# Kernel optimization log

Hardware: AMD Instinct MI355X
Metric: run time of the kernel (lower is better)

## Reference

```python
import jax, jax.numpy as jnp
import numpy as np

N = 50000          # node_num
E = 800000         # edges before self-loops (avg degree 16)
H = 1              # heads
C = 64             # out_channel (== embedding dim)
D_IN = 64          # in_channel
NEG_SLOPE = 0.2    # GraphLayer leaky_relu negative_slope
BN_EPS = 1e-5


def setup_inputs() -> dict:
    key = jax.random.key(0)
    ks = jax.random.split(key, 12)
    x = jax.random.normal(ks[0], (N, D_IN), jnp.float32)
    # random edges with no self-loops (forward removes then re-adds self-loops)
    src = jax.random.randint(ks[1], (E,), 0, N, dtype=jnp.int32)
    off = jax.random.randint(ks[2], (E,), 1, N, dtype=jnp.int32)
    dst = (src + off) % N
    edge_index = jnp.stack([src, dst])            # [2, E], row0=j (source), row1=i (target)
    embedding = jax.random.normal(ks[3], (N, C), jnp.float32)
    sc = 1.0 / np.sqrt(D_IN)
    W = jax.random.normal(ks[4], (H * C, D_IN), jnp.float32) * sc   # lin.weight
    att_i = jax.random.normal(ks[5], (1, H, C), jnp.float32) * 0.1
    att_j = jax.random.normal(ks[6], (1, H, C), jnp.float32) * 0.1
    att_em_i = jax.random.normal(ks[7], (1, H, C), jnp.float32) * 0.1
    att_em_j = jax.random.normal(ks[8], (1, H, C), jnp.float32) * 0.1
    bias = jnp.zeros((C,), jnp.float32)           # GraphLayer bias (concat=False)
    bn_gamma = jnp.ones((C,), jnp.float32)
    bn_beta = jnp.zeros((C,), jnp.float32)
    return {"x": x, "edge_index": edge_index, "embedding": embedding, "W": W,
            "att_i": att_i, "att_j": att_j, "att_em_i": att_em_i, "att_em_j": att_em_j,
            "bias": bias, "bn_gamma": bn_gamma, "bn_beta": bn_beta}


def reference(x, edge_index, embedding, W, att_i, att_j, att_em_i, att_em_j, bias, bn_gamma, bn_beta):
    n = x.shape[0]
    xl = (x @ W.T).reshape(n, H, C)                       # lin(x) -> [N, H, C]
    # add self-loops (input edges have none)
    loops = jnp.arange(n, dtype=edge_index.dtype)
    src = jnp.concatenate([edge_index[0], loops])         # j
    dst = jnp.concatenate([edge_index[1], loops])         # i (aggregation target)
    x_j = xl[src]                                         # [E', H, C]
    x_i = xl[dst]
    emb_i = embedding[dst][:, None, :]                    # [E', 1, C] broadcast over heads
    emb_j = embedding[src][:, None, :]
    # alpha = <cat(x_i, emb_i), cat(att_i, att_em_i)> + <cat(x_j, emb_j), cat(att_j, att_em_j)>
    a = ((x_i * att_i).sum(-1) + (emb_i * att_em_i).sum(-1)
         + (x_j * att_j).sum(-1) + (emb_j * att_em_j).sum(-1))   # [E', H]
    a = jnp.where(a >= 0, a, NEG_SLOPE * a)               # leaky_relu(0.2)
    # segment softmax over target nodes
    amax = jax.ops.segment_max(a, dst, num_segments=n)    # every node has a self-loop
    ea = jnp.exp(a - amax[dst])
    denom = jax.ops.segment_sum(ea, dst, num_segments=n)
    alpha = ea / (denom[dst] + 1e-16)                     # [E', H]
    msg = x_j * alpha[..., None]                          # [E', H, C]
    out = jax.ops.segment_sum(msg, dst, num_segments=n)   # [N, H, C]
    out = out.mean(axis=1) + bias                         # concat=False -> head mean
    # BatchNorm1d (training mode: batch stats) + ReLU
    mu = out.mean(axis=0)
    var = ((out - mu) ** 2).mean(axis=0)
    out = (out - mu) * jax.lax.rsqrt(var + BN_EPS) * bn_gamma + bn_beta
    return jnp.maximum(out, 0.0)
```

## Files before the change

### kernel.cpp

```cpp
#include <hip/hip_runtime.h>
#include <hip/hip_bf16.h>

#define NEG_SLOPE 0.2f
#define BN_EPS 1e-5f
#define CAP 48
#define NGRP 391
#define NSLICE 782
#define PER 1024
#define SLICELEN 1024

typedef __attribute__((ext_vector_type(8))) short bf16x8;
typedef __attribute__((ext_vector_type(4))) float f32x4;
typedef __attribute__((ext_vector_type(4))) int i32x4;

__device__ __forceinline__ bf16x8 pk8(float4 a, float4 b) {
    union { __hip_bfloat16 h; short s; } u;
    bf16x8 r;
    u.h = __float2bfloat16(a.x); r[0] = u.s;
    u.h = __float2bfloat16(a.y); r[1] = u.s;
    u.h = __float2bfloat16(a.z); r[2] = u.s;
    u.h = __float2bfloat16(a.w); r[3] = u.s;
    u.h = __float2bfloat16(b.x); r[4] = u.s;
    u.h = __float2bfloat16(b.y); r[5] = u.s;
    u.h = __float2bfloat16(b.z); r[6] = u.s;
    u.h = __float2bfloat16(b.w); r[7] = u.s;
    return r;
}

__global__ void __launch_bounds__(256, 8)
k_part_mfma(const float* __restrict__ x, const float* __restrict__ W,
            const float* __restrict__ emb,
            const float* __restrict__ att_i, const float* __restrict__ att_j,
            const float* __restrict__ att_em_i, const float* __restrict__ att_em_j,
            const int* __restrict__ src, const int* __restrict__ dst, int E,
            unsigned* __restrict__ region, unsigned short* __restrict__ start16,
            __hip_bfloat16* __restrict__ xlh, float* __restrict__ s_i,
            float* __restrict__ s_j, float* __restrict__ sums, int N) {
    __shared__ unsigned cnt[NGRP];
    __shared__ unsigned pfx[NGRP + 1];
    __shared__ unsigned run[NGRP];
    __shared__ unsigned sbuf[PER];
    int tid = threadIdx.x;
    int lane = tid & 63;
    int m = lane & 15;
    int q = lane >> 4;

    if (blockIdx.x == 0 && tid < 128) sums[tid] = 0.f;

    int gw = blockIdx.x * 4 + (tid >> 6);
    int ntiles = (N + 15) >> 4;
    int r0 = gw * 16;
    int rload = r0 + m; if (rload > N - 1) rload = N - 1;
    const float* xrow = x + (size_t)rload * 64;
    float4 xa0 = *(const float4*)(xrow + q * 8);
    float4 xa1 = *(const float4*)(xrow + q * 8 + 4);
    float4 xb0 = *(const float4*)(xrow + 32 + q * 8);
    float4 xb1 = *(const float4*)(xrow + 32 + q * 8 + 4);

    {
        int b = blockIdx.x;
        int e0 = b * PER;
        int e1 = e0 + PER; if (e1 > E) e1 = E;
        int ecnt = e1 - e0; if (ecnt < 0) ecnt = 0;
        int e4 = ecnt & ~3;
        for (int gg = tid; gg < NGRP; gg += 256) cnt[gg] = 0;
        __syncthreads();
        int o = tid * 4;
        i32x4 d4 = {0, 0, 0, 0}, s4 = d4;
        bool have = o < e4;
        if (have) {
            d4 = *(const i32x4*)(dst + e0 + o);
            s4 = *(const i32x4*)(src + e0 + o);
            atomicAdd(&cnt[d4[0] >> 7], 1u);
            atomicAdd(&cnt[d4[1] >> 7], 1u);
            atomicAdd(&cnt[d4[2] >> 7], 1u);
            atomicAdd(&cnt[d4[3] >> 7], 1u);
        }
        for (int oo = e4 + tid; oo < ecnt; oo += 256)
            atomicAdd(&cnt[dst[e0 + oo] >> 7], 1u);
        __syncthreads();
        if (tid < 64) {
            unsigned loc[7]; unsigned own = 0;
            int g0 = tid * 7;
#pragma unroll
            for (int k = 0; k < 7; ++k) {
                int g = g0 + k;
                unsigned c = (g < NGRP) ? cnt[g] : 0u;
                loc[k] = own; own += c;
            }
            unsigned incl = own;
#pragma unroll
            for (int o2 = 1; o2 < 64; o2 <<= 1) {
                unsigned t = __shfl_up(incl, o2, 64);
                if (tid >= o2) incl += t;
            }
            unsigned excl = incl - own;
#pragma unroll
            for (int k = 0; k < 7; ++k) {
                int g = g0 + k;
                if (g < NGRP) pfx[g] = excl + loc[k];
            }
            if (tid == 0) pfx[NGRP] = (unsigned)ecnt;
        }
        __syncthreads();
        for (int gg = tid; gg < NGRP; gg += 256) run[gg] = pfx[gg];
        for (int gg = tid; gg < NGRP + 1; gg += 256)
            start16[(size_t)gg * NSLICE + b] = (unsigned short)pfx[gg];
        __syncthreads();
#define PUT(dd, ss) { int g_ = (dd) >> 7; unsigned p_ = atomicAdd(&run[g_], 1u); \
        sbuf[p_] = (((unsigned)((dd) & 127)) << 16) | (unsigned)(ss); }
        if (have) {
            PUT(d4[0], s4[0])
            PUT(d4[1], s4[1])
            PUT(d4[2], s4[2])
            PUT(d4[3], s4[3])
        }
        for (int oo = e4 + tid; oo < ecnt; oo += 256) {
            int d = dst[e0 + oo]; int s = src[e0 + oo];
            PUT(d, s)
        }
#undef PUT
        __syncthreads();
        unsigned* rg = region + (size_t)b * SLICELEN;
        for (int o2 = tid * 4; o2 < ecnt; o2 += 1024)
            *(i32x4*)(rg + o2) = *(const i32x4*)(sbuf + o2);
    }

    if (gw >= ntiles) return;
    bf16x8 A0 = pk8(xa0, xa1);
    bf16x8 A1 = pk8(xb0, xb1);

    f32x4 acc0 = {0.f, 0.f, 0.f, 0.f}, acc1 = acc0, acc2 = acc0, acc3 = acc0;
#define CTILE(ct, accv) { \
        const float* wrow = W + (size_t)(ct * 16 + m) * 64; \
        float4 wb0 = *(const float4*)(wrow + q * 8); \
        float4 wb1 = *(const float4*)(wrow + q * 8 + 4); \
        float4 wb2 = *(const float4*)(wrow + 32 + q * 8); \
        float4 wb3 = *(const float4*)(wrow + 32 + q * 8 + 4); \
        bf16x8 B0 = pk8(wb0, wb1); \
        bf16x8 B1 = pk8(wb2, wb3); \
        accv = __builtin_amdgcn_mfma_f32_16x16x32_bf16(A0, B0, accv, 0, 0, 0); \
        accv = __builtin_amdgcn_mfma_f32_16x16x32_bf16(A1, B1, accv, 0, 0, 0); }
    CTILE(0, acc0) CTILE(1, acc1) CTILE(2, acc2) CTILE(3, acc3)
#undef CTILE

    float ati0 = att_i[m],    ati1 = att_i[16 + m],    ati2 = att_i[32 + m],    ati3 = att_i[48 + m];
    float atj0 = att_j[m],    atj1 = att_j[16 + m],    atj2 = att_j[32 + m],    atj3 = att_j[48 + m];
    float aei0 = att_em_i[m], aei1 = att_em_i[16 + m], aei2 = att_em_i[32 + m], aei3 = att_em_i[48 + m];
    float aej0 = att_em_j[m], aej1 = att_em_j[16 + m], aej2 = att_em_j[32 + m], aej3 = att_em_j[48 + m];
#pragma unroll
    for (int reg = 0; reg < 4; ++reg) {
        int r = r0 + q * 4 + reg;
        if (r < N) {
            float v0 = acc0[reg], v1 = acc1[reg], v2 = acc2[reg], v3 = acc3[reg];
            __hip_bfloat16* xo = xlh + (size_t)r * 64 + m;
            xo[0]  = __float2bfloat16(v0);
            xo[16] = __float2bfloat16(v1);
            xo[32] = __float2bfloat16(v2);
            xo[48] = __float2bfloat16(v3);
            const float* er = emb + (size_t)r * 64 + m;
            float e0 = er[0], e1 = er[16], e2 = er[32], e3 = er[48];
            float pi = v0 * ati0 + v1 * ati1 + v2 * ati2 + v3 * ati3
                     + e0 * aei0 + e1 * aei1 + e2 * aei2 + e3 * aei3;
            float pj = v0 * atj0 + v1 * atj1 + v2 * atj2 + v3 * atj3
                     + e0 * aej0 + e1 * aej1 + e2 * aej2 + e3 * aej3;
#pragma unroll
            for (int o = 1; o < 16; o <<= 1) {
                pi += __shfl_xor(pi, o, 64);
                pj += __shfl_xor(pj, o, 64);
            }
            if (m == 0) { s_i[r] = pi; s_j[r] = pj; }
        }
    }
}

__global__ void __launch_bounds__(512, 4)
k_bucket(const unsigned* __restrict__ region, const unsigned short* __restrict__ start16,
         const float* __restrict__ s_j, uint2* __restrict__ bucket,
         int* __restrict__ cursor, int N) {
    __shared__ int ldeg[128];
    int tid = threadIdx.x;
    int g = blockIdx.x;
    if (tid < 128) ldeg[tid] = 0;
    __syncthreads();
    const unsigned short* s0row = start16 + (size_t)g * NSLICE;
    const unsigned short* s1row = s0row + NSLICE;
    for (int b = tid; b < NSLICE; b += 512) {
        unsigned st0 = s0row[b];
        unsigned st1 = s1row[b];
        const unsigned* rg = region + (size_t)b * SLICELEN;
        for (unsigned i = st0; i < st1; ++i) {
            unsigned e = rg[i];
            int dlo = e >> 16;
            int s = (int)(e & 0xffffu);
            float sj = s_j[s];
            int p = atomicAdd(&ldeg[dlo], 1);
            if (p < CAP) {
                uint2 ent;
                ent.x = (unsigned)s;
                ent.y = __float_as_uint(sj);
                bucket[((size_t)(g << 7) + dlo) * CAP + p] = ent;
            }
        }
    }
    __syncthreads();
    if (tid < 128) {
        int node = (g << 7) + tid;
        if (node < N) cursor[node] = ldeg[tid];
    }
}

__global__ void __launch_bounds__(256, 8)
k_aggregate(const __hip_bfloat16* __restrict__ xlh, const float* __restrict__ s_i,
            const float* __restrict__ s_j, const int* __restrict__ cursor,
            const uint2* __restrict__ bucket, const float* __restrict__ bias,
            __hip_bfloat16* __restrict__ preh, int N) {
    int lane = threadIdx.x & 63;
    int w = threadIdx.x >> 6;
    int i = blockIdx.x * 4 + w;
    if (i >= N) return;

    size_t base = (size_t)i * CAP;
    uint2 ent = {0u, 0u};
    if (lane < CAP) ent = bucket[base + lane];
    int deg = cursor[i];
    float sii = s_i[i];
    float sji = s_j[i];
    float selfx = (float)xlh[(size_t)i * 64 + lane];
    float bi = bias[lane];

    deg = deg < CAP ? deg : CAP;
    float araw = sii + __uint_as_float(ent.y);
    araw = araw >= 0.f ? araw : NEG_SLOPE * araw;
    float eraw = __expf(araw);
    bool valid = lane < deg;
    int jreg = valid ? (int)ent.x : 0;
    float wreg = valid ? eraw : 0.f;

    float a_self = sii + sji;
    a_self = a_self >= 0.f ? a_self : NEG_SLOPE * a_self;
    float w_self = __expf(a_self);
    float dsum = wreg;
#pragma unroll
    for (int o = 32; o; o >>= 1) dsum += __shfl_xor(dsum, o, 64);

    float acc = w_self * selfx;
    int wbits = __float_as_int(wreg);
    int nb = (deg + 15) >> 4;
#define GL(k) int j##k = __builtin_amdgcn_readlane(jreg, e + k); \
              float u##k = __int_as_float(__builtin_amdgcn_readlane(wbits, e + k)); \
              float v##k = (float)xlh[(size_t)j##k * 64 + lane];
#define FM(k) acc = fmaf(u##k, v##k, acc);
    for (int b = 0; b < nb; ++b) {
        int e = b << 4;
        GL(0) GL(1) GL(2) GL(3) GL(4) GL(5) GL(6) GL(7)
        GL(8) GL(9) GL(10) GL(11) GL(12) GL(13) GL(14) GL(15)
        FM(0) FM(1) FM(2) FM(3) FM(4) FM(5) FM(6) FM(7)
        FM(8) FM(9) FM(10) FM(11) FM(12) FM(13) FM(14) FM(15)
    }
#undef GL
#undef FM
    float denom = dsum + w_self + 1e-16f;
    preh[(size_t)i * 64 + lane] = __float2bfloat16(acc / denom + bi);
}

__global__ void k_stats(const __hip_bfloat16* __restrict__ preh, int N,
                        float* __restrict__ sums) {
    int lane = threadIdx.x & 63, w = threadIdx.x >> 6;
    int gwave = blockIdx.x * (blockDim.x >> 6) + w;
    int stride = gridDim.x * (blockDim.x >> 6);
    float s = 0.f, q = 0.f;
    for (int r = gwave; r < N; r += stride) {
        float v = (float)preh[(size_t)r * 64 + lane];
        s += v;
        q = fmaf(v, v, q);
    }
    __shared__ float ls[4][64], lq[4][64];
    ls[w][lane] = s;
    lq[w][lane] = q;
    __syncthreads();
    if (w == 0) {
        s = ls[0][lane] + ls[1][lane] + ls[2][lane] + ls[3][lane];
        q = lq[0][lane] + lq[1][lane] + lq[2][lane] + lq[3][lane];
        atomicAdd(&sums[lane], s);
        atomicAdd(&sums[64 + lane], q);
    }
}

__global__ void __launch_bounds__(256, 4)
k_norm(const __hip_bfloat16* __restrict__ preh, const float* __restrict__ sums,
       const float* __restrict__ gamma, const float* __restrict__ beta,
       float* __restrict__ out, int N, int total4) {
    __shared__ float sc_sh[64], sh_sh[64];
    int tid = threadIdx.x;
    if (tid < 64) {
        float invN = 1.f / (float)N;
        float mu = sums[tid] * invN;
        float var = sums[64 + tid] * invN - mu * mu;
        float sc = gamma[tid] * rsqrtf(var + BN_EPS);
        sc_sh[tid] = sc;
        sh_sh[tid] = beta[tid] - mu * sc;
    }
    __syncthreads();
    typedef __attribute__((ext_vector_type(4))) short s16x4;
    union { s16x4 v; short s[4]; } u;
    for (int i = blockIdx.x * blockDim.x + tid; i < total4; i += gridDim.x * blockDim.x) {
        int c = (i & 15) * 4;
        u.v = ((const s16x4*)preh)[i];
        float4 r;
        union { __hip_bfloat16 h; short s; } cv;
        cv.s = u.s[0]; r.x = fmaxf(fmaf((float)cv.h, sc_sh[c + 0], sh_sh[c + 0]), 0.f);
        cv.s = u.s[1]; r.y = fmaxf(fmaf((float)cv.h, sc_sh[c + 1], sh_sh[c + 1]), 0.f);
        cv.s = u.s[2]; r.z = fmaxf(fmaf((float)cv.h, sc_sh[c + 2], sh_sh[c + 2]), 0.f);
        cv.s = u.s[3]; r.w = fmaxf(fmaf((float)cv.h, sc_sh[c + 3], sh_sh[c + 3]), 0.f);
        ((float4*)out)[i] = r;
    }
}

extern "C" void kernel_launch(void* const* d_in, const int* in_sizes, int n_in,
                              void* d_out, int out_size, void* d_ws, size_t ws_size,
                              hipStream_t stream) {
    const float* x        = (const float*)d_in[0];
    const int*   ei       = (const int*)d_in[1];
    const float* emb      = (const float*)d_in[2];
    const float* W        = (const float*)d_in[3];
    const float* att_i    = (const float*)d_in[4];
    const float* att_j    = (const float*)d_in[5];
    const float* att_em_i = (const float*)d_in[6];
    const float* att_em_j = (const float*)d_in[7];
    const float* bias     = (const float*)d_in[8];
    const float* gamma    = (const float*)d_in[9];
    const float* beta     = (const float*)d_in[10];

    int N = in_sizes[0] / 64;
    int E = in_sizes[1] / 2;
    const int* srcv = ei;
    const int* dstv = ei + E;

    char* ws = (char*)d_ws;
    size_t o = 0;
    auto alloc = [&](size_t bytes) -> char* {
        char* p = ws + o;
        o += bytes;
        o = (o + 255) & ~(size_t)255;
        return p;
    };
    __hip_bfloat16* xlh     = (__hip_bfloat16*)alloc((size_t)N * 64 * 2);
    __hip_bfloat16* preh    = (__hip_bfloat16*)alloc((size_t)N * 64 * 2);
    float* s_i              = (float*)alloc((size_t)N * 4);
    float* s_j              = (float*)alloc((size_t)N * 4);
    uint2* bucket           = (uint2*)alloc((size_t)N * CAP * 8);
    int* cursor             = (int*)alloc((size_t)N * 4);
    unsigned* region        = (unsigned*)alloc((size_t)NSLICE * SLICELEN * 4);
    unsigned short* start16 = (unsigned short*)alloc((size_t)(NGRP + 1) * NSLICE * 2);
    float* sums             = (float*)alloc(128 * 4);

    int nslice = (E + PER - 1) / PER;
    k_part_mfma<<<nslice, 256, 0, stream>>>(x, W, emb, att_i, att_j, att_em_i,
                                            att_em_j, srcv, dstv, E, region, start16,
                                            xlh, s_i, s_j, sums, N);
    k_bucket<<<NGRP, 512, 0, stream>>>(region, start16, s_j, bucket, cursor, N);
    k_aggregate<<<(N + 3) / 4, 256, 0, stream>>>(xlh, s_i, s_j, cursor, bucket,
                                                 bias, preh, N);
    k_stats<<<256, 256, 0, stream>>>(preh, N, sums);
    int total4 = N * 16;
    k_norm<<<1024, 256, 0, stream>>>(preh, sums, gamma, beta, (float*)d_out, N, total4);
}
```

Baseline: 165.8 us.

## Gather neighbor rows with 16-byte vector loads across 8 edges per wave

```diff
diff --git a/kernel.cpp b/kernel.cpp
--- a/kernel.cpp
+++ b/kernel.cpp
@@ -25,6 +25,12 @@
     u.h = __float2bfloat16(b.z); r[6] = u.s;
     u.h = __float2bfloat16(b.w); r[7] = u.s;
     return r;
+}
+
+__device__ __forceinline__ float bf2f(short s) {
+    union { __hip_bfloat16 h; short s; } u;
+    u.s = s;
+    return (float)u.h;
 }
 
 __global__ void __launch_bounds__(256, 8)
@@ -219,6 +225,8 @@
     int w = threadIdx.x >> 6;
     int i = blockIdx.x * 4 + w;
     if (i >= N) return;
+    int sc = lane & 7;
+    int se = lane >> 3;
 
     size_t base = (size_t)i * CAP;
     uint2 ent = {0u, 0u};
@@ -226,8 +234,7 @@
     int deg = cursor[i];
     float sii = s_i[i];
     float sji = s_j[i];
-    float selfx = (float)xlh[(size_t)i * 64 + lane];
-    float bi = bias[lane];
+    bf16x8 selfv = *(const bf16x8*)((const short*)xlh + (size_t)i * 64 + sc * 8);
 
     deg = deg < CAP ? deg : CAP;
     float araw = sii + __uint_as_float(ent.y);
@@ -243,25 +250,39 @@
     float dsum = wreg;
 #pragma unroll
     for (int o = 32; o; o >>= 1) dsum += __shfl_xor(dsum, o, 64);
-
-    float acc = w_self * selfx;
+    float denom = dsum + w_self + 1e-16f;
+
+    float acc8[8];
+    float us = (se == 0) ? w_self : 0.f;
+#pragma unroll
+    for (int c = 0; c < 8; ++c) acc8[c] = us * bf2f(selfv[c]);
+
     int wbits = __float_as_int(wreg);
-    int nb = (deg + 15) >> 4;
-#define GL(k) int j##k = __builtin_amdgcn_readlane(jreg, e + k); \
-              float u##k = __int_as_float(__builtin_amdgcn_readlane(wbits, e + k)); \
-              float v##k = (float)xlh[(size_t)j##k * 64 + lane];
-#define FM(k) acc = fmaf(u##k, v##k, acc);
-    for (int b = 0; b < nb; ++b) {
-        int e = b << 4;
-        GL(0) GL(1) GL(2) GL(3) GL(4) GL(5) GL(6) GL(7)
-        GL(8) GL(9) GL(10) GL(11) GL(12) GL(13) GL(14) GL(15)
-        FM(0) FM(1) FM(2) FM(3) FM(4) FM(5) FM(6) FM(7)
-        FM(8) FM(9) FM(10) FM(11) FM(12) FM(13) FM(14) FM(15)
-    }
-#undef GL
-#undef FM
-    float denom = dsum + w_self + 1e-16f;
-    preh[(size_t)i * 64 + lane] = __float2bfloat16(acc / denom + bi);
+    int nb8 = (deg + 7) >> 3;
+    for (int b = 0; b < nb8; ++b) {
+        int e = (b << 3) + se;
+        int j = __shfl(jreg, e, 64);
+        float u = __int_as_float(__shfl(wbits, e, 64));
+        bf16x8 v = *(const bf16x8*)((const short*)xlh + (size_t)j * 64 + sc * 8);
+#pragma unroll
+        for (int c = 0; c < 8; ++c) acc8[c] = fmaf(u, bf2f(v[c]), acc8[c]);
+    }
+#pragma unroll
+    for (int off = 8; off < 64; off <<= 1) {
+#pragma unroll
+        for (int c = 0; c < 8; ++c) acc8[c] += __shfl_xor(acc8[c], off, 64);
+    }
+    if (se == 0) {
+        union { __hip_bfloat16 h; short s; } cv;
+        bf16x8 r;
+#pragma unroll
+        for (int c = 0; c < 8; ++c) {
+            float rv = acc8[c] / denom + bias[sc * 8 + c];
+            cv.h = __float2bfloat16(rv);
+            r[c] = cv.s;
+        }
+        *(bf16x8*)((short*)preh + (size_t)i * 64 + sc * 8) = r;
+    }
 }
 
 __global__ void k_stats(const __hip_bfloat16* __restrict__ preh, int N,
```

Result: no change. 166.6 us (+0.5%).
